# Kernel optimization log

Hardware: AMD Instinct MI355X
Metric: run time of the kernel (lower is better)

Reference implementation:

```python
import jax, jax.numpy as jnp
import numpy as np

B, S, D = 4, 4096, 512      # batch, seq_len, data_embedding_size
FH = 2048                    # forecasting_hidden_size
H = 64                       # lstm_hidden_size (proj_size=1 since H>1)


def setup_inputs() -> dict:
    key = jax.random.key(0)
    ks = jax.random.split(key, 10)
    sD, sFH, sH = 1.0 / np.sqrt(D), 1.0 / np.sqrt(FH), 1.0 / np.sqrt(H)
    return {
        "x": jax.random.normal(ks[0], (B, S, D), dtype=jnp.float32),
        # forecasting head: Linear(D->FH) then Linear(FH->D)
        "W1": jax.random.uniform(ks[1], (FH, D), minval=-sD, maxval=sD),
        "b1": jax.random.uniform(ks[2], (FH,), minval=-sD, maxval=sD),
        "W2": jax.random.uniform(ks[3], (D, FH), minval=-sFH, maxval=sFH),
        "b2": jax.random.uniform(ks[4], (D,), minval=-sFH, maxval=sFH),
        # LSTM (1 layer, proj_size=1): gate order i,f,g,o
        "Wih": jax.random.uniform(ks[5], (4 * H, D), minval=-sH, maxval=sH),
        "Whh": jax.random.uniform(ks[6], (4 * H, 1), minval=-sH, maxval=sH),  # recurrent input is projected h (size 1)
        "bih": jax.random.uniform(ks[7], (4 * H,), minval=-sH, maxval=sH),
        "bhh": jax.random.uniform(ks[8], (4 * H,), minval=-sH, maxval=sH),
        "Whr": jax.random.uniform(ks[9], (1, H), minval=-sH, maxval=sH),  # projection h_inner -> h
    }


def reference(x, W1, b1, W2, b2, Wih, Whh, bih, bhh, Whr):
    Bx, Sx, Dx = x.shape
    flat = x.reshape(-1, Dx)                       # [B*S, D]
    fore = (flat @ W1.T + b1) @ W2.T + b2          # [B*S, D]  (two linears, no activation)

    # Original code loops i in range(S) over the FLATTENED sequence -> only first S tokens.
    xs = flat[:Sx]
    fs = fore[:Sx]

    def cell(h, c, inp):
        # gates = W_ih x + b_ih + W_hh h + b_hh ; PyTorch order i,f,g,o
        g = Wih @ inp + bih + Whh @ h + bhh        # [4H]
        i, f, gg, o = jnp.split(g, 4)
        c2 = jax.nn.sigmoid(f) * c + jax.nn.sigmoid(i) * jnp.tanh(gg)
        h2 = Whr @ (jax.nn.sigmoid(o) * jnp.tanh(c2))   # projected hidden, shape [1]
        return h2, c2

    def step(carry, tok):
        h, c = carry
        xt, ft = tok
        h2, c2 = cell(h, c, xt)        # real token: updates state
        hf, _ = cell(h2, c2, ft)       # forecasted token: peeks, does not update state
        return (h2, c2), (h2[0], hf[0])

    init = (jnp.zeros((1,), x.dtype), jnp.zeros((H,), x.dtype))
    _, (p, pf) = jax.lax.scan(step, init, (xs, fs))   # p, pf: [S]

    progress = jnp.broadcast_to(p[None, :], (Bx, Sx))
    forecasted_progress = jnp.broadcast_to(pf[None, :], (Bx, Sx))
    return progress, forecasted_progress, fore.reshape(1, -1, Dx)
```

## Files before the change

### kernel.cpp

```cpp
#include <hip/hip_runtime.h>
#include <hip/hip_bf16.h>


#if __has_builtin(__builtin_amdgcn_exp2f)
__device__ __forceinline__ float EXP2(float x) { return __builtin_amdgcn_exp2f(x); }
#else
__device__ __forceinline__ float EXP2(float x) { return __expf(x * 0.6931471805599453f); }
#endif
#if __has_builtin(__builtin_amdgcn_rcpf)
__device__ __forceinline__ float RCPF(float x) { return __builtin_amdgcn_rcpf(x); }
#else
__device__ __forceinline__ float RCPF(float x) { return 1.0f / x; }
#endif

constexpr float L2E  = 1.4426950408889634f;
constexpr float L2E2 = 2.8853900817779268f;

__device__ __forceinline__ float sig_f(float x)  { return RCPF(1.0f + EXP2(-L2E * x)); }
__device__ __forceinline__ float tanh_f(float x) { return fmaf(-2.0f, RCPF(1.0f + EXP2(L2E2 * x)), 1.0f); }

template<int CTRL>
__device__ __forceinline__ float dppadd(float x) {
    return x + __int_as_float(__builtin_amdgcn_update_dpp(
        0, __float_as_int(x), CTRL, 0xf, 0xf, true));
}
__device__ __forceinline__ float dpp_sum64_lane63(float x) {
    x = dppadd<0x111>(x); x = dppadd<0x112>(x); x = dppadd<0x114>(x);
    x = dppadd<0x118>(x); x = dppadd<0x142>(x); x = dppadd<0x143>(x);
    return x;
}
__device__ __forceinline__ float readlane63(float x) {
    return __int_as_float(__builtin_amdgcn_readlane(__float_as_int(x), 63));
}
__device__ __forceinline__ float readlane_s(float x, int s) {
    return __int_as_float(__builtin_amdgcn_readlane(__float_as_int(x), s));
}

using bf16x8 = __attribute__((ext_vector_type(8))) __bf16;
using f32x4  = __attribute__((ext_vector_type(4))) float;

__device__ __forceinline__ void mfma_tile128_lds(
    const __hip_bfloat16* __restrict__ A, int lda,
    const __hip_bfloat16* __restrict__ B, int ldb,
    int K, int bm, int bn,
    const float* __restrict__ bias,
    float* __restrict__ Cf, int ldc,
    __hip_bfloat16* __restrict__ Cb,
    __hip_bfloat16* __restrict__ Ct, int ldt,
    __hip_bfloat16* __restrict__ Bs)
{
    const int tid  = threadIdx.x;
    const int w    = tid >> 6;
    const int lane = tid & 63;
    const int rc   = lane & 15;
    const int kg   = lane >> 4;
    const __hip_bfloat16* ap0 = A + (size_t)(bm + w * 16 + rc) * lda + kg * 8;
    const __hip_bfloat16* ap1 = ap0 + (size_t)64 * lda;

#define LD8(P) (*reinterpret_cast<const bf16x8*>(P))
    const f32x4 z{0.f, 0.f, 0.f, 0.f};
    f32x4 c00 = z, c01 = z, c02 = z, c03 = z;
    f32x4 c10 = z, c11 = z, c12 = z, c13 = z;

    for (int kb = 0; kb < K; kb += 512) {
        __syncthreads();
        #pragma unroll
        for (int i = 0; i < 16; ++i) {
            const int G = i * 256 + tid;
            const int row = G >> 6, kc = G & 63;
            const bf16x8 v = LD8(B + (size_t)(bn + row) * ldb + kb + kc * 8);
            *reinterpret_cast<bf16x8*>(Bs + row * 512 + ((kc ^ (row & 7)) << 3)) = v;
        }
        __syncthreads();

        bf16x8 a0 = LD8(ap0 + kb), a1 = LD8(ap1 + kb);
        #pragma unroll 4
        for (int s = 0; s < 16; ++s) {
            bf16x8 a0n = a0, a1n = a1;
            if (s < 15) {
                a0n = LD8(ap0 + kb + (s + 1) * 32);
                a1n = LD8(ap1 + kb + (s + 1) * 32);
            }
            bf16x8 bf[4];
            #pragma unroll
            for (int g = 0; g < 4; ++g) {
                const int row = g * 16 + rc;
                const int off = row * 512 + (((s * 4 + kg) ^ (row & 7)) << 3);
                bf[g] = *reinterpret_cast<const bf16x8*>(Bs + off);
            }
            c00 = __builtin_amdgcn_mfma_f32_16x16x32_bf16(a0, bf[0], c00, 0, 0, 0);
            c01 = __builtin_amdgcn_mfma_f32_16x16x32_bf16(a0, bf[1], c01, 0, 0, 0);
            c02 = __builtin_amdgcn_mfma_f32_16x16x32_bf16(a0, bf[2], c02, 0, 0, 0);
            c03 = __builtin_amdgcn_mfma_f32_16x16x32_bf16(a0, bf[3], c03, 0, 0, 0);
            c10 = __builtin_amdgcn_mfma_f32_16x16x32_bf16(a1, bf[0], c10, 0, 0, 0);
            c11 = __builtin_amdgcn_mfma_f32_16x16x32_bf16(a1, bf[1], c11, 0, 0, 0);
            c12 = __builtin_amdgcn_mfma_f32_16x16x32_bf16(a1, bf[2], c12, 0, 0, 0);
            c13 = __builtin_amdgcn_mfma_f32_16x16x32_bf16(a1, bf[3], c13, 0, 0, 0);
            a0 = a0n; a1 = a1n;
        }
    }
#undef LD8

    const int row0 = bm + w * 16 + kg * 4;
    const int colb = bn + rc;
#define EPI(ACC, HOFF, CT) {                                                  \
        const int col = colb + (CT) * 16;                                     \
        const float bb = bias ? bias[col] : 0.0f;                             \
        _Pragma("unroll")                                                     \
        for (int i = 0; i < 4; ++i) {                                         \
            const float v = (ACC)[i] + bb;                                    \
            const int row = row0 + (HOFF) + i;                                \
            if (Cf) Cf[(size_t)row * ldc + col] = v;                          \
            if (Cb) Cb[(size_t)row * ldc + col] = __float2bfloat16(v);        \
            if (Ct) Ct[(size_t)col * ldt + row] = __float2bfloat16(v);        \
        }}
    EPI(c00, 0, 0)  EPI(c01, 0, 1)  EPI(c02, 0, 2)  EPI(c03, 0, 3)
    EPI(c10, 64, 0) EPI(c11, 64, 1) EPI(c12, 64, 2) EPI(c13, 64, 3)
#undef EPI
}

__global__ __launch_bounds__(256) void convA_kernel(
    const float* __restrict__ W2, const float* __restrict__ W1,
    const float* __restrict__ Wih,
    const float* __restrict__ bih, const float* __restrict__ bhh,
    __hip_bfloat16* __restrict__ W2b, __hip_bfloat16* __restrict__ W1t,
    __hip_bfloat16* __restrict__ Wihb, float* __restrict__ gxbias)
{
    const int bid = blockIdx.x, tid = threadIdx.x;
#define CVT4(SRC, DST, BASE) {                                                \
        const size_t i = ((size_t)(BASE) * 256 + tid) * 4;                    \
        const float4 v = *reinterpret_cast<const float4*>((SRC) + i);         \
        __hip_bfloat16 o[4] = {__float2bfloat16(v.x), __float2bfloat16(v.y),  \
                               __float2bfloat16(v.z), __float2bfloat16(v.w)}; \
        *reinterpret_cast<ushort4*>((DST) + i) =                              \
            *reinterpret_cast<const ushort4*>(o); }
    if (bid < 1024) {
        CVT4(W2, W2b, bid)
    } else if (bid < 1280) {
        __shared__ float lds[64][65];
        const int b = bid - 1024;
        const int br = b >> 3, bc = b & 7;
        const int r0 = tid >> 4, c4 = (tid & 15) * 4;
        #pragma unroll
        for (int u = 0; u < 4; ++u) {
            const int row = r0 + u * 16;
            const float4 v = *reinterpret_cast<const float4*>(
                &W1[(size_t)(br * 64 + row) * 512 + bc * 64 + c4]);
            lds[row][c4 + 0] = v.x; lds[row][c4 + 1] = v.y;
            lds[row][c4 + 2] = v.z; lds[row][c4 + 3] = v.w;
        }
        __syncthreads();
        const int jj0 = tid >> 4, kk4 = (tid & 15) * 4;
        #pragma unroll
        for (int u = 0; u < 4; ++u) {
            const int jj = jj0 + u * 16;
            __hip_bfloat16 o[4] = {
                __float2bfloat16(lds[kk4 + 0][jj]), __float2bfloat16(lds[kk4 + 1][jj]),
                __float2bfloat16(lds[kk4 + 2][jj]), __float2bfloat16(lds[kk4 + 3][jj])};
            *reinterpret_cast<ushort4*>(
                &W1t[(size_t)(bc * 64 + jj) * 2048 + br * 64 + kk4]) =
                *reinterpret_cast<const ushort4*>(o);
        }
    } else if (bid < 1408) {
        CVT4(Wih, Wihb, bid - 1280)
    } else {
        gxbias[tid] = bih[tid] + bhh[tid];
    }
#undef CVT4
}

__global__ __launch_bounds__(256) void convB_kernel(
    const float* __restrict__ x, const float* __restrict__ W2,
    const float* __restrict__ b1, const float* __restrict__ b2,
    const __hip_bfloat16* __restrict__ W2b, const __hip_bfloat16* __restrict__ W1t,
    __hip_bfloat16* __restrict__ xb,
    __hip_bfloat16* __restrict__ Weffb, __hip_bfloat16* __restrict__ WeffTb,
    float* __restrict__ beff)
{
    __shared__ __hip_bfloat16 Bs[64 * 512];
    const int bid = blockIdx.x, tid = threadIdx.x;
    if (bid < 32) {
        const int bm = (bid >> 3) * 128, bn = (bid & 7) * 64;
        mfma_tile128_lds(W2b, 2048, W1t, 2048, 2048, bm, bn, nullptr,
                         nullptr, 512, Weffb, WeffTb, 512, Bs);
    } else if (bid < 40) {
        const int w = tid >> 6, j = tid & 63;
        const int base = (bid - 32) * 64 + w * 16;
        for (int o = 0; o < 16; ++o) {
            const int i = base + o;
            float s = 0.0f;
            #pragma unroll
            for (int m = 0; m < 32; ++m)
                s = fmaf(W2[(size_t)i * 2048 + j + 64 * m], b1[j + 64 * m], s);
            s = dpp_sum64_lane63(s);
            if (j == 63) beff[i] = s + b2[i];
        }
    } else {
        const int b = bid - 40;
        const float4* src = reinterpret_cast<const float4*>(x) + (size_t)b * 1024;
        ushort4* dst = reinterpret_cast<ushort4*>(xb) + (size_t)b * 1024;
        float4 v[4];
        #pragma unroll
        for (int u = 0; u < 4; ++u) v[u] = src[u * 256 + tid];
        #pragma unroll
        for (int u = 0; u < 4; ++u) {
            __hip_bfloat16 o[4] = {__float2bfloat16(v[u].x), __float2bfloat16(v[u].y),
                                   __float2bfloat16(v[u].z), __float2bfloat16(v[u].w)};
            dst[u * 256 + tid] = *reinterpret_cast<const ushort4*>(o);
        }
    }
}

__global__ __launch_bounds__(256) void wggx_kernel(
    const __hip_bfloat16* __restrict__ Wihb, const __hip_bfloat16* __restrict__ WeffTb,
    const __hip_bfloat16* __restrict__ xb,
    const float* __restrict__ Wih, const float* __restrict__ beff,
    const float* __restrict__ gxbias,
    __hip_bfloat16* __restrict__ Wgb, float* __restrict__ bf2,
    float* __restrict__ Gx)
{
    __shared__ __hip_bfloat16 Bs[64 * 512];
    const int bid = blockIdx.x;
    if (bid < 16) {
        const int bm = (bid >> 3) * 128, bn = (bid & 7) * 64;
        mfma_tile128_lds(Wihb, 512, WeffTb, 512, 512, bm, bn, nullptr,
                         nullptr, 512, Wgb, nullptr, 0, Bs);
    } else if (bid == 16) {
        const int w = threadIdx.x >> 6, j = threadIdx.x & 63;
        for (int o = 0; o < 64; ++o) {
            const int i = w * 64 + o;
            float s = 0.0f;
            #pragma unroll
            for (int m = 0; m < 8; ++m)
                s = fmaf(Wih[(size_t)i * 512 + j + 64 * m], beff[j + 64 * m], s);
            s = dpp_sum64_lane63(s);
            if (j == 63) bf2[i] = s;
        }
    } else {
        const int b = bid - 17;
        const int bm = (b >> 2) * 128, bn = (b & 3) * 64;
        mfma_tile128_lds(xb, 512, Wihb, 512, 512, bm, bn, gxbias,
                         Gx, 256, nullptr, nullptr, 0, Bs);
    }
}

__global__ __launch_bounds__(256) void fused_kernel(
    int phase, int first, int last,
    int fore_cnt, int gf_cnt,
    const __hip_bfloat16* __restrict__ xb, const __hip_bfloat16* __restrict__ Weffb,
    const __hip_bfloat16* __restrict__ Wgb_in,
    const float* __restrict__ beff, const float* __restrict__ bf2,
    const float* __restrict__ Gx, float* __restrict__ Gf,
    const float* __restrict__ Gf_in, const float* __restrict__ gxbias,
    const float* __restrict__ Whh, const float* __restrict__ Whr,
    const float* __restrict__ hprev, float* __restrict__ hnext,
    float* __restrict__ P, float* __restrict__ Q,
    float* __restrict__ fore, float* __restrict__ out)
{
    __shared__ __hip_bfloat16 Bs[64 * 512];
    constexpr int CH = 32;
    constexpr int S = 4096, BS = 4 * 4096;

    if (blockIdx.x < 32) {
        const int chunk = blockIdx.x * 4 + (threadIdx.x >> 6);
        const int j = threadIdx.x & 63;
        const float wi = Whh[j], wf = Whh[64 + j];
        const float wg2 = Whh[128 + j], wo = Whh[192 + j];
        const float* ab = Gx + (size_t)chunk * CH * 256 + j;

        float hp = 0.0f;
        if (!first) {
            const int idx = chunk * CH - 1 + j;
            hp = (idx >= 0 && idx < S) ? hprev[idx] : 0.0f;
        }

        if (phase == 0) {
            float Pv = 1.0f, Qv = 0.0f;
            #pragma unroll 8
            for (int s = 0; s < CH; ++s) {
                const float hs = first ? 0.0f : readlane_s(hp, s);
                const float ai = ab[s * 256]       + wi  * hs;
                const float af = ab[s * 256 + 64]  + wf  * hs;
                const float ag = ab[s * 256 + 128] + wg2 * hs;
                const float si = sig_f(ai);
                const float sf = sig_f(af);
                const float tg = tanh_f(ag);
                Pv = sf * Pv;
                Qv = fmaf(sf, Qv, si * tg);
            }
            P[chunk * 64 + j] = Pv;
            Q[chunk * 64 + j] = Qv;
        } else {
            const float whr = Whr[j];
            float c = 0.0f;
            #pragma unroll 8
            for (int m = 0; m < chunk; ++m)
                c = fmaf(P[m * 64 + j], c, Q[m * 64 + j]);
            float vp = 0.0f, vpf = 0.0f;
            const float* gfp = Gf_in ? Gf_in + (size_t)chunk * CH * 256 + j : nullptr;
            const float bi0 = gxbias[j],        bi1 = gxbias[64 + j];
            const float bi2 = gxbias[128 + j],  bi3 = gxbias[192 + j];
            #pragma unroll 4
            for (int s = 0; s < CH; ++s) {
                const float hs = first ? 0.0f : readlane_s(hp, s);
                const float ai = ab[s * 256]       + wi  * hs;
                const float af = ab[s * 256 + 64]  + wf  * hs;
                const float ag = ab[s * 256 + 128] + wg2 * hs;
                const float ao = ab[s * 256 + 192] + wo  * hs;
                const float si = sig_f(ai);
                const float sf = sig_f(af);
                const float tg = tanh_f(ag);
                const float so = sig_f(ao);
                c = fmaf(sf, c, si * tg);
                const float tc = tanh_f(c);
                float hv = tc * (so * whr);
                hv = dpp_sum64_lane63(hv);
                const float hn = readlane63(hv);
                vp = (j == s) ? hn : vp;
                if (last) {
                    const float fi = gfp[s * 256]       + bi0 + wi  * hn;
                    const float ff = gfp[s * 256 + 64]  + bi1 + wf  * hn;
                    const float fg = gfp[s * 256 + 128] + bi2 + wg2 * hn;
                    const float fo = gfp[s * 256 + 192] + bi3 + wo  * hn;
                    const float cf = sig_f(ff) * c + sig_f(fi) * tanh_f(fg);
                    float hf = sig_f(fo) * tanh_f(cf) * whr;
                    hf = dpp_sum64_lane63(hf);
                    const float hfn = readlane63(hf);
                    vpf = (j == s) ? hfn : vpf;
                }
            }
            if (j < CH) {
                const int t = chunk * CH + j;
                if (last) {
                    #pragma unroll
                    for (int b = 0; b < 4; ++b) {
                        out[b * S + t]      = vp;
                        out[BS + b * S + t] = vpf;
                    }
                } else {
                    hnext[t] = vp;
                }
            }
        }
        return;
    }

    const int bt = blockIdx.x - 32;
    if (bt < fore_cnt) {
        const int tile = (bt & 7) * 128 + (bt >> 3);
        const int bm = (tile >> 3) * 128, bn = (tile & 7) * 64;
        mfma_tile128_lds(xb, 512, Weffb, 512, 512, bm, bn, beff,
                         fore, 512, nullptr, nullptr, 0, Bs);
    } else if (bt < fore_cnt + gf_cnt) {
        const int g = bt - fore_cnt;
        const int bm = (g >> 2) * 128, bn = (g & 3) * 64;
        mfma_tile128_lds(xb, 512, Wgb_in, 512, 512, bm, bn, bf2,
                         Gf, 256, nullptr, nullptr, 0, Bs);
    }
}

extern "C" void kernel_launch(void* const* d_in, const int* in_sizes, int n_in,
                              void* d_out, int out_size, void* d_ws, size_t ws_size,
                              hipStream_t stream) {
    const float* x   = (const float*)d_in[0];
    const float* W1  = (const float*)d_in[1];
    const float* b1  = (const float*)d_in[2];
    const float* W2  = (const float*)d_in[3];
    const float* b2  = (const float*)d_in[4];
    const float* Wih = (const float*)d_in[5];
    const float* Whh = (const float*)d_in[6];
    const float* bih = (const float*)d_in[7];
    const float* bhh = (const float*)d_in[8];
    const float* Whr = (const float*)d_in[9];
    float* out = (float*)d_out;

    constexpr int Bb = 4, S = 4096;
    const int M = Bb * S;

    float* ws      = (float*)d_ws;
    float* beff    = ws;
    float* gxbias  = beff + 512;
    float* bf2     = gxbias + 256;
    float* Gx      = bf2 + 256;
    float* Gf      = Gx + S * 256;
    float* Pp      = Gf + S * 256;
    float* Qq      = Pp + 8192;
    float* h0      = Qq + 8192;
    float* h1      = h0 + S;
    __hip_bfloat16* xb     = (__hip_bfloat16*)(h1 + S);
    __hip_bfloat16* W2b    = xb + (size_t)M * 512;
    __hip_bfloat16* W1t    = W2b + 512 * 2048;
    __hip_bfloat16* Wihb   = W1t + 512 * 2048;
    __hip_bfloat16* Weffb  = Wihb + 256 * 512;
    __hip_bfloat16* WeffTb = Weffb + 512 * 512;
    __hip_bfloat16* Wgb    = WeffTb + 512 * 512;

    float* fore = out + 2 * M;

    convA_kernel<<<1409, 256, 0, stream>>>(
        W2, W1, Wih, bih, bhh, W2b, W1t, Wihb, gxbias);

    convB_kernel<<<2088, 256, 0, stream>>>(
        x, W2, b1, b2, W2b, W1t, xb, Weffb, WeffTb, beff);

    wggx_kernel<<<145, 256, 0, stream>>>(
        Wihb, WeffTb, xb, Wih, beff, gxbias, Wgb, bf2, Gx);

    fused_kernel<<<32 + 1024, 256, 0, stream>>>(
        0, 1, 0, 1024, 0,
        xb, Weffb, Wgb, beff, bf2, Gx, Gf, nullptr, gxbias, Whh, Whr,
        h0, h0, Pp, Qq, fore, out);

    fused_kernel<<<32 + 128, 256, 0, stream>>>(
        1, 1, 0, 0, 128,
        xb, Weffb, Wgb, beff, bf2, Gx, Gf, nullptr, gxbias, Whh, Whr,
        h0, h0, Pp, Qq, fore, out);

    fused_kernel<<<32, 256, 0, stream>>>(
        0, 0, 0, 0, 0,
        xb, Weffb, Wgb, beff, bf2, Gx, Gf, nullptr, gxbias, Whh, Whr,
        h0, h1, Pp, Qq, fore, out);

    fused_kernel<<<32, 256, 0, stream>>>(
        1, 0, 1, 0, 0,
        xb, Weffb, Wgb, beff, bf2, Gx, Gf, Gf, gxbias, Whh, Whr,
        h0, h1, Pp, Qq, fore, out);
}
```

Before: 152.2 us.

## Split-K the Weff GEMM and move Wg GEMM into fused kernel

```diff
diff --git a/kernel.cpp b/kernel.cpp
--- a/kernel.cpp
+++ b/kernel.cpp
@@ -173,19 +173,21 @@
     const float* __restrict__ x, const float* __restrict__ W2,
     const float* __restrict__ b1, const float* __restrict__ b2,
     const __hip_bfloat16* __restrict__ W2b, const __hip_bfloat16* __restrict__ W1t,
-    __hip_bfloat16* __restrict__ xb,
-    __hip_bfloat16* __restrict__ Weffb, __hip_bfloat16* __restrict__ WeffTb,
+    __hip_bfloat16* __restrict__ xb, float* __restrict__ Wpart,
     float* __restrict__ beff)
 {
     __shared__ __hip_bfloat16 Bs[64 * 512];
     const int bid = blockIdx.x, tid = threadIdx.x;
-    if (bid < 32) {
-        const int bm = (bid >> 3) * 128, bn = (bid & 7) * 64;
-        mfma_tile128_lds(W2b, 2048, W1t, 2048, 2048, bm, bn, nullptr,
-                         nullptr, 512, Weffb, WeffTb, 512, Bs);
-    } else if (bid < 40) {
+    if (bid < 128) {
+        const int tile = bid >> 2, ks = bid & 3;
+        const int bm = (tile >> 3) * 128, bn = (tile & 7) * 64;
+        mfma_tile128_lds(W2b + ks * 512, 2048, W1t + ks * 512, 2048, 512,
+                         bm, bn, nullptr,
+                         Wpart + (size_t)ks * 512 * 512, 512,
+                         nullptr, nullptr, 0, Bs);
+    } else if (bid < 136) {
         const int w = tid >> 6, j = tid & 63;
-        const int base = (bid - 32) * 64 + w * 16;
+        const int base = (bid - 128) * 64 + w * 16;
         for (int o = 0; o < 16; ++o) {
             const int i = base + o;
             float s = 0.0f;
@@ -196,7 +198,7 @@
             if (j == 63) beff[i] = s + b2[i];
         }
     } else {
-        const int b = bid - 40;
+        const int b = bid - 136;
         const float4* src = reinterpret_cast<const float4*>(x) + (size_t)b * 1024;
         ushort4* dst = reinterpret_cast<ushort4*>(xb) + (size_t)b * 1024;
         float4 v[4];
@@ -212,19 +214,37 @@
 }
 
 __global__ __launch_bounds__(256) void wggx_kernel(
-    const __hip_bfloat16* __restrict__ Wihb, const __hip_bfloat16* __restrict__ WeffTb,
-    const __hip_bfloat16* __restrict__ xb,
+    const float* __restrict__ Wpart,
+    const __hip_bfloat16* __restrict__ Wihb, const __hip_bfloat16* __restrict__ xb,
     const float* __restrict__ Wih, const float* __restrict__ beff,
     const float* __restrict__ gxbias,
-    __hip_bfloat16* __restrict__ Wgb, float* __restrict__ bf2,
-    float* __restrict__ Gx)
+    __hip_bfloat16* __restrict__ Weffb, __hip_bfloat16* __restrict__ WeffTb,
+    float* __restrict__ bf2, float* __restrict__ Gx)
 {
     __shared__ __hip_bfloat16 Bs[64 * 512];
     const int bid = blockIdx.x;
     if (bid < 16) {
-        const int bm = (bid >> 3) * 128, bn = (bid & 7) * 64;
-        mfma_tile128_lds(Wihb, 512, WeffTb, 512, 512, bm, bn, nullptr,
-                         nullptr, 512, Wgb, nullptr, 0, Bs);
+        const int tid = threadIdx.x;
+        constexpr int NF4 = 512 * 512 / 4;
+        for (int u = 0; u < 16; ++u) {
+            const int g = (bid * 16 + u) * 256 + tid;
+            if (g >= NF4) break;
+            f32x4 s = *reinterpret_cast<const f32x4*>(Wpart + (size_t)g * 4);
+            #pragma unroll
+            for (int p = 1; p < 4; ++p) {
+                const f32x4 v = *reinterpret_cast<const f32x4*>(
+                    Wpart + (size_t)p * 512 * 512 + (size_t)g * 4);
+                s[0] += v[0]; s[1] += v[1]; s[2] += v[2]; s[3] += v[3];
+            }
+            const int row = (g * 4) >> 9, col = (g * 4) & 511;
+            __hip_bfloat16 o[4] = {__float2bfloat16(s[0]), __float2bfloat16(s[1]),
+                                   __float2bfloat16(s[2]), __float2bfloat16(s[3])};
+            *reinterpret_cast<ushort4*>(Weffb + (size_t)row * 512 + col) =
+                *reinterpret_cast<const ushort4*>(o);
+            #pragma unroll
+            for (int e = 0; e < 4; ++e)
+                WeffTb[(size_t)(col + e) * 512 + row] = o[e];
+        }
     } else if (bid == 16) {
         const int w = threadIdx.x >> 6, j = threadIdx.x & 63;
         for (int o = 0; o < 64; ++o) {
@@ -246,9 +266,10 @@
 
 __global__ __launch_bounds__(256) void fused_kernel(
     int phase, int first, int last,
-    int fore_cnt, int gf_cnt,
+    int wg_cnt, int fore_cnt, int gf_cnt,
     const __hip_bfloat16* __restrict__ xb, const __hip_bfloat16* __restrict__ Weffb,
-    const __hip_bfloat16* __restrict__ Wgb_in,
+    const __hip_bfloat16* __restrict__ WeffTb, const __hip_bfloat16* __restrict__ Wihb,
+    __hip_bfloat16* __restrict__ Wgb, const __hip_bfloat16* __restrict__ Wgb_in,
     const float* __restrict__ beff, const float* __restrict__ bf2,
     const float* __restrict__ Gx, float* __restrict__ Gf,
     const float* __restrict__ Gf_in, const float* __restrict__ gxbias,
@@ -346,13 +367,18 @@
     }
 
     const int bt = blockIdx.x - 32;
-    if (bt < fore_cnt) {
-        const int tile = (bt & 7) * 128 + (bt >> 3);
+    if (bt < wg_cnt) {
+        const int bm = (bt >> 3) * 128, bn = (bt & 7) * 64;
+        mfma_tile128_lds(Wihb, 512, WeffTb, 512, 512, bm, bn, nullptr,
+                         nullptr, 512, Wgb, nullptr, 0, Bs);
+    } else if (bt < wg_cnt + fore_cnt) {
+        const int f = bt - wg_cnt;
+        const int tile = (f & 7) * 128 + (f >> 3);
         const int bm = (tile >> 3) * 128, bn = (tile & 7) * 64;
         mfma_tile128_lds(xb, 512, Weffb, 512, 512, bm, bn, beff,
                          fore, 512, nullptr, nullptr, 0, Bs);
-    } else if (bt < fore_cnt + gf_cnt) {
-        const int g = bt - fore_cnt;
+    } else if (bt < wg_cnt + fore_cnt + gf_cnt) {
+        const int g = bt - wg_cnt - fore_cnt;
         const int bm = (g >> 2) * 128, bn = (g & 3) * 64;
         mfma_tile128_lds(xb, 512, Wgb_in, 512, 512, bm, bn, bf2,
                          Gf, 256, nullptr, nullptr, 0, Bs);
@@ -387,7 +413,8 @@
     float* Qq      = Pp + 8192;
     float* h0      = Qq + 8192;
     float* h1      = h0 + S;
-    __hip_bfloat16* xb     = (__hip_bfloat16*)(h1 + S);
+    float* Wpart   = h1 + S;
+    __hip_bfloat16* xb     = (__hip_bfloat16*)(Wpart + 4 * 512 * 512);
     __hip_bfloat16* W2b    = xb + (size_t)M * 512;
     __hip_bfloat16* W1t    = W2b + 512 * 2048;
     __hip_bfloat16* Wihb   = W1t + 512 * 2048;
@@ -400,29 +427,33 @@
     convA_kernel<<<1409, 256, 0, stream>>>(
         W2, W1, Wih, bih, bhh, W2b, W1t, Wihb, gxbias);
 
-    convB_kernel<<<2088, 256, 0, stream>>>(
-        x, W2, b1, b2, W2b, W1t, xb, Weffb, WeffTb, beff);
+    convB_kernel<<<128 + 8 + 2048, 256, 0, stream>>>(
+        x, W2, b1, b2, W2b, W1t, xb, Wpart, beff);
 
     wggx_kernel<<<145, 256, 0, stream>>>(
-        Wihb, WeffTb, xb, Wih, beff, gxbias, Wgb, bf2, Gx);
-
-    fused_kernel<<<32 + 1024, 256, 0, stream>>>(
-        0, 1, 0, 1024, 0,
-        xb, Weffb, Wgb, beff, bf2, Gx, Gf, nullptr, gxbias, Whh, Whr,
+        Wpart, Wihb, xb, Wih, beff, gxbias, Weffb, WeffTb, bf2, Gx);
+
+    fused_kernel<<<32 + 16 + 1024, 256, 0, stream>>>(
+        0, 1, 0, 16, 1024, 0,
+        xb, Weffb, WeffTb, Wihb, Wgb, Wgb, beff, bf2,
+        Gx, Gf, nullptr, gxbias, Whh, Whr,
         h0, h0, Pp, Qq, fore, out);
 
     fused_kernel<<<32 + 128, 256, 0, stream>>>(
-        1, 1, 0, 0, 128,
-        xb, Weffb, Wgb, beff, bf2, Gx, Gf, nullptr, gxbias, Whh, Whr,
+        1, 1, 0, 0, 0, 128,
+        xb, Weffb, WeffTb, Wihb, Wgb, Wgb, beff, bf2,
+        Gx, Gf, nullptr, gxbias, Whh, Whr,
         h0, h0, Pp, Qq, fore, out);
 
     fused_kernel<<<32, 256, 0, stream>>>(
-        0, 0, 0, 0, 0,
-        xb, Weffb, Wgb, beff, bf2, Gx, Gf, nullptr, gxbias, Whh, Whr,
+        0, 0, 0, 0, 0, 0,
+        xb, Weffb, WeffTb, Wihb, Wgb, Wgb, beff, bf2,
+        Gx, Gf, nullptr, gxbias, Whh, Whr,
         h0, h1, Pp, Qq, fore, out);
 
     fused_kernel<<<32, 256, 0, stream>>>(
-        1, 0, 1, 0, 0,
-        xb, Weffb, Wgb, beff, bf2, Gx, Gf, Gf, gxbias, Whh, Whr,
+        1, 0, 1, 0, 0, 0,
+        xb, Weffb, WeffTb, Wihb, Wgb, Wgb, beff, bf2,
+        Gx, Gf, Gf, gxbias, Whh, Whr,
         h0, h1, Pp, Qq, fore, out);
 }
```

Measured after the change: 140.7 us. 7.6% less time.

## Split-K the Weff GEMM and compute Gf from bf16 fore instead of Wg

Applied to the files above, without the earlier changes.

```diff
diff --git a/kernel.cpp b/kernel.cpp
--- a/kernel.cpp
+++ b/kernel.cpp
@@ -46,7 +46,6 @@
     const float* __restrict__ bias,
     float* __restrict__ Cf, int ldc,
     __hip_bfloat16* __restrict__ Cb,
-    __hip_bfloat16* __restrict__ Ct, int ldt,
     __hip_bfloat16* __restrict__ Bs)
 {
     const int tid  = threadIdx.x;
@@ -112,7 +111,6 @@
             const int row = row0 + (HOFF) + i;                                \
             if (Cf) Cf[(size_t)row * ldc + col] = v;                          \
             if (Cb) Cb[(size_t)row * ldc + col] = __float2bfloat16(v);        \
-            if (Ct) Ct[(size_t)col * ldt + row] = __float2bfloat16(v);        \
         }}
     EPI(c00, 0, 0)  EPI(c01, 0, 1)  EPI(c02, 0, 2)  EPI(c03, 0, 3)
     EPI(c10, 64, 0) EPI(c11, 64, 1) EPI(c12, 64, 2) EPI(c13, 64, 3)
@@ -123,8 +121,10 @@
     const float* __restrict__ W2, const float* __restrict__ W1,
     const float* __restrict__ Wih,
     const float* __restrict__ bih, const float* __restrict__ bhh,
+    const float* __restrict__ b1, const float* __restrict__ b2,
     __hip_bfloat16* __restrict__ W2b, __hip_bfloat16* __restrict__ W1t,
-    __hip_bfloat16* __restrict__ Wihb, float* __restrict__ gxbias)
+    __hip_bfloat16* __restrict__ Wihb, float* __restrict__ gxbias,
+    float* __restrict__ beff)
 {
     const int bid = blockIdx.x, tid = threadIdx.x;
 #define CVT4(SRC, DST, BASE) {                                                \
@@ -163,29 +163,11 @@
         }
     } else if (bid < 1408) {
         CVT4(Wih, Wihb, bid - 1280)
+    } else if (bid == 1408) {
+        gxbias[tid] = bih[tid] + bhh[tid];
     } else {
-        gxbias[tid] = bih[tid] + bhh[tid];
-    }
-#undef CVT4
-}
-
-__global__ __launch_bounds__(256) void convB_kernel(
-    const float* __restrict__ x, const float* __restrict__ W2,
-    const float* __restrict__ b1, const float* __restrict__ b2,
-    const __hip_bfloat16* __restrict__ W2b, const __hip_bfloat16* __restrict__ W1t,
-    __hip_bfloat16* __restrict__ xb,
-    __hip_bfloat16* __restrict__ Weffb, __hip_bfloat16* __restrict__ WeffTb,
-    float* __restrict__ beff)
-{
-    __shared__ __hip_bfloat16 Bs[64 * 512];
-    const int bid = blockIdx.x, tid = threadIdx.x;
-    if (bid < 32) {
-        const int bm = (bid >> 3) * 128, bn = (bid & 7) * 64;
-        mfma_tile128_lds(W2b, 2048, W1t, 2048, 2048, bm, bn, nullptr,
-                         nullptr, 512, Weffb, WeffTb, 512, Bs);
-    } else if (bid < 40) {
         const int w = tid >> 6, j = tid & 63;
-        const int base = (bid - 32) * 64 + w * 16;
+        const int base = (bid - 1409) * 64 + w * 16;
         for (int o = 0; o < 16; ++o) {
             const int i = base + o;
             float s = 0.0f;
@@ -195,8 +177,25 @@
             s = dpp_sum64_lane63(s);
             if (j == 63) beff[i] = s + b2[i];
         }
+    }
+#undef CVT4
+}
+
+__global__ __launch_bounds__(256) void convB_kernel(
+    const float* __restrict__ x,
+    const __hip_bfloat16* __restrict__ W2b, const __hip_bfloat16* __restrict__ W1t,
+    __hip_bfloat16* __restrict__ xb, float* __restrict__ Wpart)
+{
+    __shared__ __hip_bfloat16 Bs[64 * 512];
+    const int bid = blockIdx.x, tid = threadIdx.x;
+    if (bid < 128) {
+        const int tile = bid >> 2, ks = bid & 3;
+        const int bm = (tile >> 3) * 128, bn = (tile & 7) * 64;
+        mfma_tile128_lds(W2b + ks * 512, 2048, W1t + ks * 512, 2048, 512,
+                         bm, bn, nullptr,
+                         Wpart + (size_t)ks * 512 * 512, 512, nullptr, Bs);
     } else {
-        const int b = bid - 40;
+        const int b = bid - 128;
         const float4* src = reinterpret_cast<const float4*>(x) + (size_t)b * 1024;
         ushort4* dst = reinterpret_cast<ushort4*>(xb) + (size_t)b * 1024;
         float4 v[4];
@@ -212,35 +211,34 @@
 }
 
 __global__ __launch_bounds__(256) void wggx_kernel(
-    const __hip_bfloat16* __restrict__ Wihb, const __hip_bfloat16* __restrict__ WeffTb,
-    const __hip_bfloat16* __restrict__ xb,
-    const float* __restrict__ Wih, const float* __restrict__ beff,
+    const float* __restrict__ Wpart,
+    const __hip_bfloat16* __restrict__ Wihb, const __hip_bfloat16* __restrict__ xb,
     const float* __restrict__ gxbias,
-    __hip_bfloat16* __restrict__ Wgb, float* __restrict__ bf2,
-    float* __restrict__ Gx)
+    __hip_bfloat16* __restrict__ Weffb, float* __restrict__ Gx)
 {
     __shared__ __hip_bfloat16 Bs[64 * 512];
     const int bid = blockIdx.x;
     if (bid < 16) {
-        const int bm = (bid >> 3) * 128, bn = (bid & 7) * 64;
-        mfma_tile128_lds(Wihb, 512, WeffTb, 512, 512, bm, bn, nullptr,
-                         nullptr, 512, Wgb, nullptr, 0, Bs);
-    } else if (bid == 16) {
-        const int w = threadIdx.x >> 6, j = threadIdx.x & 63;
-        for (int o = 0; o < 64; ++o) {
-            const int i = w * 64 + o;
-            float s = 0.0f;
+        const int tid = threadIdx.x;
+        for (int u = 0; u < 16; ++u) {
+            const int g = (bid * 16 + u) * 256 + tid;
+            f32x4 s = *reinterpret_cast<const f32x4*>(Wpart + (size_t)g * 4);
             #pragma unroll
-            for (int m = 0; m < 8; ++m)
-                s = fmaf(Wih[(size_t)i * 512 + j + 64 * m], beff[j + 64 * m], s);
-            s = dpp_sum64_lane63(s);
-            if (j == 63) bf2[i] = s;
+            for (int p = 1; p < 4; ++p) {
+                const f32x4 v = *reinterpret_cast<const f32x4*>(
+                    Wpart + (size_t)p * 512 * 512 + (size_t)g * 4);
+                s[0] += v[0]; s[1] += v[1]; s[2] += v[2]; s[3] += v[3];
+            }
+            __hip_bfloat16 o[4] = {__float2bfloat16(s[0]), __float2bfloat16(s[1]),
+                                   __float2bfloat16(s[2]), __float2bfloat16(s[3])};
+            *reinterpret_cast<ushort4*>(Weffb + (size_t)g * 4) =
+                *reinterpret_cast<const ushort4*>(o);
         }
     } else {
-        const int b = bid - 17;
+        const int b = bid - 16;
         const int bm = (b >> 2) * 128, bn = (b & 3) * 64;
         mfma_tile128_lds(xb, 512, Wihb, 512, 512, bm, bn, gxbias,
-                         Gx, 256, nullptr, nullptr, 0, Bs);
+                         Gx, 256, nullptr, Bs);
     }
 }
 
@@ -248,8 +246,9 @@
     int phase, int first, int last,
     int fore_cnt, int gf_cnt,
     const __hip_bfloat16* __restrict__ xb, const __hip_bfloat16* __restrict__ Weffb,
-    const __hip_bfloat16* __restrict__ Wgb_in,
-    const float* __restrict__ beff, const float* __restrict__ bf2,
+    const __hip_bfloat16* __restrict__ Wihb, const __hip_bfloat16* __restrict__ foreb_in,
+    __hip_bfloat16* __restrict__ foreb_out,
+    const float* __restrict__ beff,
     const float* __restrict__ Gx, float* __restrict__ Gf,
     const float* __restrict__ Gf_in, const float* __restrict__ gxbias,
     const float* __restrict__ Whh, const float* __restrict__ Whr,
@@ -350,12 +349,12 @@
         const int tile = (bt & 7) * 128 + (bt >> 3);
         const int bm = (tile >> 3) * 128, bn = (tile & 7) * 64;
         mfma_tile128_lds(xb, 512, Weffb, 512, 512, bm, bn, beff,
-                         fore, 512, nullptr, nullptr, 0, Bs);
+                         fore, 512, (bm < 4096) ? foreb_out : nullptr, Bs);
     } else if (bt < fore_cnt + gf_cnt) {
         const int g = bt - fore_cnt;
         const int bm = (g >> 2) * 128, bn = (g & 3) * 64;
-        mfma_tile128_lds(xb, 512, Wgb_in, 512, 512, bm, bn, bf2,
-                         Gf, 256, nullptr, nullptr, 0, Bs);
+        mfma_tile128_lds(foreb_in, 512, Wihb, 512, 512, bm, bn, nullptr,
+                         Gf, 256, nullptr, Bs);
     }
 }
 
@@ -380,49 +379,52 @@
     float* ws      = (float*)d_ws;
     float* beff    = ws;
     float* gxbias  = beff + 512;
-    float* bf2     = gxbias + 256;
-    float* Gx      = bf2 + 256;
+    float* Gx      = gxbias + 256;
     float* Gf      = Gx + S * 256;
     float* Pp      = Gf + S * 256;
     float* Qq      = Pp + 8192;
     float* h0      = Qq + 8192;
     float* h1      = h0 + S;
-    __hip_bfloat16* xb     = (__hip_bfloat16*)(h1 + S);
+    float* Wpart   = h1 + S;
+    __hip_bfloat16* xb     = (__hip_bfloat16*)(Wpart + 4 * 512 * 512);
     __hip_bfloat16* W2b    = xb + (size_t)M * 512;
     __hip_bfloat16* W1t    = W2b + 512 * 2048;
     __hip_bfloat16* Wihb   = W1t + 512 * 2048;
     __hip_bfloat16* Weffb  = Wihb + 256 * 512;
-    __hip_bfloat16* WeffTb = Weffb + 512 * 512;
-    __hip_bfloat16* Wgb    = WeffTb + 512 * 512;
+    __hip_bfloat16* foreb  = Weffb + 512 * 512;
 
     float* fore = out + 2 * M;
 
-    convA_kernel<<<1409, 256, 0, stream>>>(
-        W2, W1, Wih, bih, bhh, W2b, W1t, Wihb, gxbias);
-
-    convB_kernel<<<2088, 256, 0, stream>>>(
-        x, W2, b1, b2, W2b, W1t, xb, Weffb, WeffTb, beff);
-
-    wggx_kernel<<<145, 256, 0, stream>>>(
-        Wihb, WeffTb, xb, Wih, beff, gxbias, Wgb, bf2, Gx);
+    convA_kernel<<<1417, 256, 0, stream>>>(
+        W2, W1, Wih, bih, bhh, b1, b2, W2b, W1t, Wihb, gxbias, beff);
+
+    convB_kernel<<<128 + 2048, 256, 0, stream>>>(
+        x, W2b, W1t, xb, Wpart);
+
+    wggx_kernel<<<144, 256, 0, stream>>>(
+        Wpart, Wihb, xb, gxbias, Weffb, Gx);
 
     fused_kernel<<<32 + 1024, 256, 0, stream>>>(
         0, 1, 0, 1024, 0,
-        xb, Weffb, Wgb, beff, bf2, Gx, Gf, nullptr, gxbias, Whh, Whr,
+        xb, Weffb, Wihb, foreb, foreb, beff,
+        Gx, Gf, nullptr, gxbias, Whh, Whr,
         h0, h0, Pp, Qq, fore, out);
 
     fused_kernel<<<32 + 128, 256, 0, stream>>>(
         1, 1, 0, 0, 128,
-        xb, Weffb, Wgb, beff, bf2, Gx, Gf, nullptr, gxbias, Whh, Whr,
+        xb, Weffb, Wihb, foreb, foreb, beff,
+        Gx, Gf, nullptr, gxbias, Whh, Whr,
         h0, h0, Pp, Qq, fore, out);
 
     fused_kernel<<<32, 256, 0, stream>>>(
         0, 0, 0, 0, 0,
-        xb, Weffb, Wgb, beff, bf2, Gx, Gf, nullptr, gxbias, Whh, Whr,
+        xb, Weffb, Wihb, foreb, foreb, beff,
+        Gx, Gf, nullptr, gxbias, Whh, Whr,
         h0, h1, Pp, Qq, fore, out);
 
     fused_kernel<<<32, 256, 0, stream>>>(
         1, 0, 1, 0, 0,
-        xb, Weffb, Wgb, beff, bf2, Gx, Gf, Gf, gxbias, Whh, Whr,
+        xb, Weffb, Wihb, foreb, foreb, beff,
+        Gx, Gf, Gf, gxbias, Whh, Whr,
         h0, h1, Pp, Qq, fore, out);
 }
```

New measurement: 130.2 us. 1.17x faster.
